# Kernel tuning notes

Measured on AMD Instinct MI355X. Metric: run time of the kernel, lower is better.

Reference implementation:

```python
import jax, jax.numpy as jnp
import numpy as np

EPS = 1e-12


def setup_inputs() -> dict:
    key = jax.random.key(0)
    k1, k2, k3 = jax.random.split(key, 3)
    N, H, W, D, K = 32, 64, 64, 512, 116
    x = jax.random.normal(k1, (N, H, W, D), dtype=jnp.float32)
    conv_w = jax.random.normal(k2, (D, K), dtype=jnp.float32) * 0.05
    C = jax.random.normal(k3, (D, K), dtype=jnp.float32) * 0.05
    return {"x": x, "conv_w": conv_w, "C": C}


def reference(x, conv_w, C):
    # x: (N,H,W,D); conv_w: (D,K) 1x1-conv kernel; C: (D,K) cluster centers.
    # Assignment logits via 1x1 conv == matmul over channels.
    s = jnp.einsum('nhwd,dk->nhwk', x, conv_w)          # (N,H,W,K)
    a = jax.nn.softmax(s, axis=-1)                      # softmax over clusters
    # Algebraic decomposition of sum_{h,w} a[...,k] * (x[...,d] + C[d,k]):
    ax = jnp.einsum('nhwk,nhwd->ndk', a, x)             # (N,D,K)
    asum = jnp.sum(a, axis=(1, 2))                      # (N,K)
    v = ax + C[None, :, :] * asum[:, None, :]           # (N,D,K)
    # Intra-normalization: after transpose to (N,K,D) the norm is over D.
    v = v / jnp.sqrt(jnp.sum(v * v, axis=1, keepdims=True) + EPS)
    # Flatten in (N, D, K) row-major order (matches tf transpose-back + Flatten).
    v = v.reshape(v.shape[0], -1)                       # (N, D*K)
    v = v / jnp.sqrt(jnp.sum(v * v, axis=-1, keepdims=True) + EPS)
    return v
```

## Files before the change

kernel.cpp:

```cpp
#include <hip/hip_runtime.h>
#include <hip/hip_bf16.h>

#define EPS_F 1e-12f

typedef __attribute__((ext_vector_type(8))) short bf16x8;
typedef __attribute__((ext_vector_type(4))) float f32x4;

__device__ __forceinline__ unsigned short f2bf(float f) {
    __hip_bfloat16 h = __float2bfloat16(f);
    unsigned short u; __builtin_memcpy(&u, &h, 2); return u;
}


__global__ void wt_prep(const float* __restrict__ w,
                        unsigned short* __restrict__ WT) {
    int id = blockIdx.x * 256 + threadIdx.x;
    int k = id >> 9, d = id & 511;
    WT[k * 512 + d] = (k < 116) ? f2bf(w[d * 116 + k]) : (unsigned short)0;
}

__global__ __launch_bounds__(256, 2)
void assign_k(const float* __restrict__ x,
              const unsigned short* __restrict__ WT,
              unsigned short* __restrict__ At,
              float* __restrict__ asum) {
    __shared__ unsigned short sm[27648];
    unsigned short* Xs = sm;
    unsigned short* Ws = sm + 18432;
    const int tid = threadIdx.x;
    const int wave = tid >> 6, lane = tid & 63;
    const int quad = lane >> 4, l15 = lane & 15;
    const int pxbase = blockIdx.x * 256;
    const int n = pxbase >> 12;

    f32x4 acc[4][8];
#pragma unroll
    for (int s = 0; s < 4; ++s)
#pragma unroll
        for (int c = 0; c < 8; ++c) acc[s][c] = (f32x4){0.f, 0.f, 0.f, 0.f};

    for (int dch = 0; dch < 8; ++dch) {
        const int dof = dch * 64;
#pragma unroll
        for (int it = 0; it < 16; ++it) {
            int cid = it * 256 + tid;
            int r = cid >> 4, co = (cid & 15) * 4;
            float4 v = *(const float4*)(x + (size_t)(pxbase + r) * 512 + dof + co);
            ushort4 u;
            u.x = f2bf(v.x); u.y = f2bf(v.y); u.z = f2bf(v.z); u.w = f2bf(v.w);
            *(ushort4*)(Xs + r * 72 + co) = u;
        }
#pragma unroll
        for (int i = 0; i < 4; ++i) {
            int cid = i * 256 + tid;
            int r = cid >> 3, co = (cid & 7) * 8;
            uint4 v = *(const uint4*)(WT + r * 512 + dof + co);
            *(uint4*)(Ws + r * 72 + co) = v;
        }
        __syncthreads();
#pragma unroll
        for (int ks = 0; ks < 2; ++ks) {
            const int ko = ks * 32 + quad * 8;
            bf16x8 af[4], bfr[8];
#pragma unroll
            for (int s = 0; s < 4; ++s)
                af[s] = *(const bf16x8*)(Xs + (wave * 64 + s * 16 + l15) * 72 + ko);
#pragma unroll
            for (int c = 0; c < 8; ++c)
                bfr[c] = *(const bf16x8*)(Ws + (c * 16 + l15) * 72 + ko);
#pragma unroll
            for (int s = 0; s < 4; ++s)
#pragma unroll
                for (int c = 0; c < 8; ++c)
                    acc[s][c] = __builtin_amdgcn_mfma_f32_16x16x32_bf16(
                        af[s], bfr[c], acc[s][c], 0, 0, 0);
        }
        __syncthreads();
    }

    const bool v7 = (l15 < 4);
#pragma unroll
    for (int s = 0; s < 4; ++s) {
#pragma unroll
        for (int r = 0; r < 4; ++r) {
            float mx = acc[s][0][r];
#pragma unroll
            for (int c = 1; c < 7; ++c) mx = fmaxf(mx, acc[s][c][r]);
            if (v7) mx = fmaxf(mx, acc[s][7][r]);
#pragma unroll
            for (int off = 1; off < 16; off <<= 1) mx = fmaxf(mx, __shfl_xor(mx, off));
            float sum = 0.f;
#pragma unroll
            for (int c = 0; c < 8; ++c) {
                float e = (c < 7 || v7) ? __expf(acc[s][c][r] - mx) : 0.f;
                acc[s][c][r] = e; sum += e;
            }
#pragma unroll
            for (int off = 1; off < 16; off <<= 1) sum += __shfl_xor(sum, off);
            float inv = 1.0f / sum;
#pragma unroll
            for (int c = 0; c < 8; ++c) acc[s][c][r] *= inv;
        }
    }

#pragma unroll
    for (int c = 0; c < 8; ++c) {
        float cs = 0.f;
#pragma unroll
        for (int s = 0; s < 4; ++s)
#pragma unroll
            for (int r = 0; r < 4; ++r) cs += acc[s][c][r];
        cs += __shfl_xor(cs, 16);
        cs += __shfl_xor(cs, 32);
        int k = c * 16 + l15;
        if (lane < 16 && k < 116) atomicAdd(asum + n * 128 + k, cs);
    }

    __syncthreads();
    unsigned short* tb = sm + wave * 4608;
    const int pw = (pxbase & 4095) + wave * 64;
#pragma unroll
    for (int ch = 0; ch < 2; ++ch) {
#pragma unroll
        for (int c4 = 0; c4 < 4; ++c4) {
            int c = ch * 4 + c4;
            int kk = c4 * 16 + l15;
#pragma unroll
            for (int s = 0; s < 4; ++s) {
                ushort4 u;
                u.x = f2bf(acc[s][c][0]); u.y = f2bf(acc[s][c][1]);
                u.z = f2bf(acc[s][c][2]); u.w = f2bf(acc[s][c][3]);
                *(ushort4*)(tb + kk * 72 + s * 16 + quad * 4) = u;
            }
        }
#pragma unroll
        for (int it = 0; it < 8; ++it) {
            int id = it * 64 + lane;
            int row = id >> 3, chk = id & 7;
            uint4 v = *(const uint4*)(tb + row * 72 + chk * 8);
            *(uint4*)(At + (size_t)(n * 128 + ch * 64 + row) * 4096 + pw + chk * 8) = v;
        }
    }
}

__global__ __launch_bounds__(256, 2)
void ax_k(const float* __restrict__ x,
          const unsigned short* __restrict__ At,
          float* __restrict__ ax0, float* __restrict__ ax1) {
    __shared__ unsigned short sm[13824];
    unsigned short* Ats = sm;
    unsigned short* Xts = sm + 9216;
    const int tid = threadIdx.x;
    const int wave = tid >> 6, lane = tid & 63;
    const int quad = lane >> 4, l15 = lane & 15;
    const int bid = blockIdx.x;
    const int xcd = bid & 7, slot = bid >> 3;
    const int dblk = slot & 7, ghi = slot >> 3;
    const int g = ghi * 8 + xcd;
    const int n = g >> 1, ps = g & 1;
    const int dbase = dblk * 64;
    const int p0 = ps * 2048;

    f32x4 acc[2][4];
#pragma unroll
    for (int s = 0; s < 2; ++s)
#pragma unroll
        for (int c = 0; c < 4; ++c) acc[s][c] = (f32x4){0.f, 0.f, 0.f, 0.f};

    for (int pc = 0; pc < 32; ++pc) {
        const int pb = p0 + pc * 64;
#pragma unroll
        for (int i = 0; i < 4; ++i) {
            int cid = i * 256 + tid;
            int r = cid >> 3, co = (cid & 7) * 8;
            uint4 v = *(const uint4*)(At + (size_t)(n * 128 + r) * 4096 + pb + co);
            *(uint4*)(Ats + r * 72 + co) = v;
        }
        {
            const float* xrow = x + (size_t)(n * 4096 + pb + lane) * 512 + dbase + wave * 16;
#pragma unroll
            for (int f = 0; f < 4; ++f) {
                float4 v = *(const float4*)(xrow + f * 4);
                int dl = wave * 16 + f * 4;
                Xts[(dl + 0) * 72 + lane] = f2bf(v.x);
                Xts[(dl + 1) * 72 + lane] = f2bf(v.y);
                Xts[(dl + 2) * 72 + lane] = f2bf(v.z);
                Xts[(dl + 3) * 72 + lane] = f2bf(v.w);
            }
        }
        __syncthreads();
#pragma unroll
        for (int ks = 0; ks < 2; ++ks) {
            const int ko = ks * 32 + quad * 8;
            bf16x8 af[2], bfr[4];
            af[0] = *(const bf16x8*)(Ats + (wave * 32 + l15) * 72 + ko);
            af[1] = *(const bf16x8*)(Ats + (wave * 32 + 16 + l15) * 72 + ko);
#pragma unroll
            for (int c = 0; c < 4; ++c)
                bfr[c] = *(const bf16x8*)(Xts + (c * 16 + l15) * 72 + ko);
#pragma unroll
            for (int s = 0; s < 2; ++s)
#pragma unroll
                for (int c = 0; c < 4; ++c)
                    acc[s][c] = __builtin_amdgcn_mfma_f32_16x16x32_bf16(
                        af[s], bfr[c], acc[s][c], 0, 0, 0);
        }
        __syncthreads();
    }

    float* axp = ps ? ax1 : ax0;
#pragma unroll
    for (int s = 0; s < 2; ++s)
#pragma unroll
        for (int c = 0; c < 4; ++c) {
            int d = dbase + c * 16 + l15;
            int k = wave * 32 + s * 16 + quad * 4;
            *(f32x4*)(axp + (size_t)(n * 512 + d) * 128 + k) = acc[s][c];
        }
}

__global__ void ss_k(const float* __restrict__ ax0, const float* __restrict__ ax1,
                     const float* __restrict__ C,
                     const float* __restrict__ asum, float* __restrict__ ssb) {
    __shared__ float red[256];
    const int tid = threadIdx.x;
    const int n = blockIdx.x >> 3, dgrp = blockIdx.x & 7;
    const int k = tid & 127, dh = tid >> 7;
    const float as = asum[n * 128 + k];
    float ssq = 0.f;
    for (int i = 0; i < 32; ++i) {
        int d = dgrp * 64 + i * 2 + dh;
        size_t ix = (size_t)(n * 512 + d) * 128 + k;
        float cc = (k < 116) ? C[d * 116 + k] : 0.f;
        float v = ax0[ix] + ax1[ix] + cc * as;
        ssq += v * v;
    }
    red[tid] = ssq;
    __syncthreads();
    if (dh == 0) atomicAdd(ssb + n * 128 + k, red[tid] + red[tid + 128]);
}

__global__ void scale_k(const float* __restrict__ ssb, float* __restrict__ scl) {
    __shared__ float red[128];
    const int n = blockIdx.x, k = threadIdx.x;
    const float s = ssb[n * 128 + k];
    red[k] = (k < 116) ? (s / (s + EPS_F)) : 0.f;
    __syncthreads();
    for (int off = 64; off > 0; off >>= 1) {
        if (k < off) red[k] += red[k + off];
        __syncthreads();
    }
    float rowinv = rsqrtf(red[0] + EPS_F);
    scl[n * 128 + k] = rsqrtf(s + EPS_F) * rowinv;
}

__global__ void emit_k(const float* __restrict__ ax0, const float* __restrict__ ax1,
                       const float* __restrict__ C,
                       const float* __restrict__ asum, const float* __restrict__ scl,
                       float* __restrict__ out) {
    const int n = blockIdx.x >> 3, dgrp = blockIdx.x & 7;
    const int tid = threadIdx.x;
    for (int i = 0; i < 29; ++i) {
        int idx = i * 256 + tid;
        int dl = idx / 116;
        int k = idx - dl * 116;
        int d = dgrp * 64 + dl;
        size_t ix = (size_t)(n * 512 + d) * 128 + k;
        float v = ax0[ix] + ax1[ix] + C[d * 116 + k] * asum[n * 128 + k];
        out[(size_t)n * 59392 + dgrp * 7424 + idx] = v * scl[n * 128 + k];
    }
}

extern "C" void kernel_launch(void* const* d_in, const int* in_sizes, int n_in,
                              void* d_out, int out_size, void* d_ws, size_t ws_size,
                              hipStream_t stream) {
    const float* x = (const float*)d_in[0];
    const float* w = (const float*)d_in[1];
    const float* C = (const float*)d_in[2];
    float* out = (float*)d_out;

    char* ws = (char*)d_ws;
    unsigned short* At  = (unsigned short*)ws;
    float* ax0  = (float*)(ws + 33554432);
    float* ax1  = (float*)(ws + 41943040);
    float* asum = (float*)(ws + 50331648);
    float* ssb  = (float*)(ws + 50348032);
    float* scl  = (float*)(ws + 50364416);
    unsigned short* WT = (unsigned short*)(ws + 50380800);

    hipMemsetAsync(ws + 50331648, 0, 32768, stream);

    wt_prep <<<256, 256, 0, stream>>>(w, WT);
    assign_k<<<512, 256, 0, stream>>>(x, WT, At, asum);
    ax_k    <<<512, 256, 0, stream>>>(x, At, ax0, ax1);
    ss_k    <<<256, 256, 0, stream>>>(ax0, ax1, C, asum, ssb);
    scale_k <<<32, 128, 0, stream>>>(ssb, scl);
    emit_k  <<<256, 256, 0, stream>>>(ax0, ax1, C, asum, scl, out);
}
```

Before: 513.7 us.

## Pre-transpose x to bf16 channel-major buffer for the aggregation GEMM

Adds a kernel that converts x to bf16 and transposes it to (N, D, pixels) layout using lane shuffles and LDS. The aggregation kernel then loads contiguous 16-byte chunks of this buffer instead of converting fp32 rows and doing scalar transposed LDS stores. It also switches the bf16 conversions to packed two-element conversions. The cost is an extra full pass over x plus a large workspace write, which adds memory traffic.

```diff
diff --git a/kernel.cpp b/kernel.cpp
--- a/kernel.cpp
+++ b/kernel.cpp
@@ -9,6 +9,11 @@
 __device__ __forceinline__ unsigned short f2bf(float f) {
     __hip_bfloat16 h = __float2bfloat16(f);
     unsigned short u; __builtin_memcpy(&u, &h, 2); return u;
+}
+__device__ __forceinline__ unsigned int pkbf(float a, float b) {
+    float2 f; f.x = a; f.y = b;
+    __hip_bfloat162 h = __float22bfloat162_rn(f);
+    unsigned int u; __builtin_memcpy(&u, &h, 4); return u;
 }
 
 
@@ -17,6 +22,55 @@
     int id = blockIdx.x * 256 + threadIdx.x;
     int k = id >> 9, d = id & 511;
     WT[k * 512 + d] = (k < 116) ? f2bf(w[d * 116 + k]) : (unsigned short)0;
+}
+
+__global__ __launch_bounds__(256, 2)
+void xt_k(const float* __restrict__ x, unsigned short* __restrict__ XT) {
+    __shared__ unsigned short XTl[512 * 70];
+    const int tid = threadIdx.x;
+    const int lane = tid & 63, w = tid >> 6;
+    const int i = (lane >> 4) & 3;
+    const int cc = lane & 15;
+    const int pxb = blockIdx.x * 64;
+    const int n = pxb >> 12, pl = pxb & 4095;
+
+    for (int it = 0; it < 32; ++it) {
+        const int dd = it >> 2, pr = it & 3;
+        const int rr = 4 * w + i;
+        const int P = pxb + pr * 16 + rr;
+        float4 X = *(const float4*)(x + (size_t)P * 512 + dd * 64 + cc * 4);
+        unsigned int u0 = pkbf(X.x, X.y), u1 = pkbf(X.z, X.w);
+        unsigned int sent = (i & 1) ? u0 : u1;
+        unsigned int got  = __shfl_xor(sent, 16);
+        unsigned int kept = (i & 1) ? u1 : u0;
+        unsigned int r0 = (i & 1) ? got : kept;
+        unsigned int r1 = (i & 1) ? kept : got;
+        unsigned int s0 = __shfl_xor(r0, 32);
+        unsigned int s1 = __shfl_xor(r1, 32);
+        unsigned int q0, q1, q2, q3;
+        if ((i >> 1) == 0) { q0 = r0; q1 = r1; q2 = s0; q3 = s1; }
+        else               { q0 = s0; q1 = s1; q2 = r0; q3 = r1; }
+        const int h = i >> 1;
+        unsigned int w0, w1;
+        if (h == 0) {
+            w0 = (q0 & 0xffffu) | (q1 << 16);
+            w1 = (q2 & 0xffffu) | (q3 << 16);
+        } else {
+            w0 = (q0 >> 16) | (q1 & 0xffff0000u);
+            w1 = (q2 >> 16) | (q3 & 0xffff0000u);
+        }
+        const int dcol = dd * 64 + cc * 4 + 2 * (i & 1) + h;
+        const int p4 = pr * 16 + 4 * w;
+        uint2 uu; uu.x = w0; uu.y = w1;
+        *(uint2*)(XTl + dcol * 70 + p4) = uu;
+    }
+    __syncthreads();
+    for (int it = 0; it < 16; ++it) {
+        int id = it * 256 + tid;
+        int row = id >> 3, ch = id & 7;
+        uint4 v = *(const uint4*)(XTl + row * 70 + ch * 8);
+        *(uint4*)(XT + ((size_t)n * 512 + row) * 4096 + pl + ch * 8) = v;
+    }
 }
 
 __global__ __launch_bounds__(256, 2)
@@ -46,9 +100,8 @@
             int cid = it * 256 + tid;
             int r = cid >> 4, co = (cid & 15) * 4;
             float4 v = *(const float4*)(x + (size_t)(pxbase + r) * 512 + dof + co);
-            ushort4 u;
-            u.x = f2bf(v.x); u.y = f2bf(v.y); u.z = f2bf(v.z); u.w = f2bf(v.w);
-            *(ushort4*)(Xs + r * 72 + co) = u;
+            uint2 u; u.x = pkbf(v.x, v.y); u.y = pkbf(v.z, v.w);
+            *(uint2*)(Xs + r * 72 + co) = u;
         }
 #pragma unroll
         for (int i = 0; i < 4; ++i) {
@@ -127,10 +180,10 @@
             int kk = c4 * 16 + l15;
 #pragma unroll
             for (int s = 0; s < 4; ++s) {
-                ushort4 u;
-                u.x = f2bf(acc[s][c][0]); u.y = f2bf(acc[s][c][1]);
-                u.z = f2bf(acc[s][c][2]); u.w = f2bf(acc[s][c][3]);
-                *(ushort4*)(tb + kk * 72 + s * 16 + quad * 4) = u;
+                uint2 u;
+                u.x = pkbf(acc[s][c][0], acc[s][c][1]);
+                u.y = pkbf(acc[s][c][2], acc[s][c][3]);
+                *(uint2*)(tb + kk * 72 + s * 16 + quad * 4) = u;
             }
         }
 #pragma unroll
@@ -144,7 +197,7 @@
 }
 
 __global__ __launch_bounds__(256, 2)
-void ax_k(const float* __restrict__ x,
+void ax_k(const unsigned short* __restrict__ XT,
           const unsigned short* __restrict__ At,
           float* __restrict__ ax0, float* __restrict__ ax1) {
     __shared__ unsigned short sm[13824];
@@ -176,17 +229,12 @@
             uint4 v = *(const uint4*)(At + (size_t)(n * 128 + r) * 4096 + pb + co);
             *(uint4*)(Ats + r * 72 + co) = v;
         }
-        {
-            const float* xrow = x + (size_t)(n * 4096 + pb + lane) * 512 + dbase + wave * 16;
-#pragma unroll
-            for (int f = 0; f < 4; ++f) {
-                float4 v = *(const float4*)(xrow + f * 4);
-                int dl = wave * 16 + f * 4;
-                Xts[(dl + 0) * 72 + lane] = f2bf(v.x);
-                Xts[(dl + 1) * 72 + lane] = f2bf(v.y);
-                Xts[(dl + 2) * 72 + lane] = f2bf(v.z);
-                Xts[(dl + 3) * 72 + lane] = f2bf(v.w);
-            }
+#pragma unroll
+        for (int i = 0; i < 2; ++i) {
+            int cid = i * 256 + tid;
+            int r = cid >> 3, co = (cid & 7) * 8;
+            uint4 v = *(const uint4*)(XT + ((size_t)n * 512 + dbase + r) * 4096 + pb + co);
+            *(uint4*)(Xts + r * 72 + co) = v;
         }
         __syncthreads();
 #pragma unroll
@@ -280,19 +328,21 @@
     float* out = (float*)d_out;
 
     char* ws = (char*)d_ws;
-    unsigned short* At  = (unsigned short*)ws;
-    float* ax0  = (float*)(ws + 33554432);
-    float* ax1  = (float*)(ws + 41943040);
-    float* asum = (float*)(ws + 50331648);
-    float* ssb  = (float*)(ws + 50348032);
-    float* scl  = (float*)(ws + 50364416);
-    unsigned short* WT = (unsigned short*)(ws + 50380800);
-
-    hipMemsetAsync(ws + 50331648, 0, 32768, stream);
+    unsigned short* XT  = (unsigned short*)ws;
+    unsigned short* At  = (unsigned short*)(ws + 134217728);
+    float* ax0  = (float*)(ws + 167772160);
+    float* ax1  = (float*)(ws + 176160768);
+    float* asum = (float*)(ws + 184549376);
+    float* ssb  = (float*)(ws + 184565760);
+    float* scl  = (float*)(ws + 184582144);
+    unsigned short* WT = (unsigned short*)(ws + 184598528);
+
+    hipMemsetAsync(ws + 184549376, 0, 32768, stream);
 
     wt_prep <<<256, 256, 0, stream>>>(w, WT);
+    xt_k    <<<2048, 256, 0, stream>>>(x, XT);
     assign_k<<<512, 256, 0, stream>>>(x, WT, At, asum);
-    ax_k    <<<512, 256, 0, stream>>>(x, At, ax0, ax1);
+    ax_k    <<<512, 256, 0, stream>>>(XT, At, ax0, ax1);
     ss_k    <<<256, 256, 0, stream>>>(ax0, ax1, C, asum, ssb);
     scale_k <<<32, 128, 0, stream>>>(ssb, scl);
     emit_k  <<<256, 256, 0, stream>>>(ax0, ax1, C, asum, scl, out);
```

Measured after the change: 613.7 us. 19.5% more time.
